# Performance work log

Measured on AMD Instinct MI355X. Metric: run time of the kernel, lower is better.

Reference implementation:

```python
import jax, jax.numpy as jnp
import numpy as np

T = 200000
N_LIMBS = 49
N_POINTS = 50
N_BONES = 20
EPS = 1e-10
REG_RATES = (0.001, 0.1)
# binary-tree skeleton: child b has parent (b-1)//2, bone-length index (b-1)%N_BONES
STRUCTURE = [((b - 1) // 2, b, (b - 1) % N_BONES) for b in range(1, N_POINTS)]

def _path_matrix():
    # P[b, i] = 1 if limb i lies on the root->node-b path. Then node position =
    # root + deltas @ P.T, which is exactly the sequential tree accumulation
    # x[b] = x[a] + delta_i of the original torch loop, vectorized.
    P = np.zeros((N_POINTS, N_LIMBS), dtype=np.float32)
    for i, (a, b, l) in enumerate(STRUCTURE):
        P[b] = P[a]
        P[b, i] = 1.0
    return P

PATH_T = jnp.asarray(_path_matrix().T)  # (n_limbs, n_points)
BONE_IDX = jnp.asarray(np.array([l for (_, _, l) in STRUCTURE], dtype=np.int32))


def setup_inputs() -> dict:
    key = jax.random.key(0)
    ks = jax.random.split(key, 10)
    f = jnp.float32
    return {
        "lines": jax.random.normal(ks[0], (N_BONES,), f) * 0.1,
        "rootsx": jax.random.normal(ks[1], (T, 1), f),
        "rootsy": jax.random.normal(ks[2], (T, 1), f),
        "rootsz": jax.random.normal(ks[3], (T, 1), f),
        "anglesx": jax.random.normal(ks[4], (T, N_LIMBS), f),
        "anglesy": jax.random.normal(ks[5], (T, N_LIMBS), f),
        "anglesz": jax.random.normal(ks[6], (T, N_LIMBS), f),
        "tarx_values": jax.random.normal(ks[7], (T, N_POINTS), f),
        "tary_values": jax.random.normal(ks[8], (T, N_POINTS), f),
        "w_values": jax.random.uniform(ks[9], (T, N_POINTS), f),
    }


def reference(lines, rootsx, rootsy, rootsz, anglesx, anglesy, anglesz,
              tarx_values, tary_values, w_values):
    # per-limb bone length L = exp(lines[l])  -> (n_limbs,)
    L = jnp.exp(lines)[BONE_IDX]
    normA = jnp.sqrt(anglesx ** 2 + anglesy ** 2 + anglesz ** 2) + EPS  # (T, n_limbs)
    dx = L * anglesx / normA
    dy = L * anglesy / normA
    dz = L * anglesz / normA
    # accumulate deltas along root->node paths (equivalent to the torch tree loop)
    x = rootsx + dx @ PATH_T  # (T, n_points); node 0 column is just the root
    y = rootsy + dy @ PATH_T
    z = rootsz + dz @ PATH_T
    loss = jnp.sum(w_values * (x - tarx_values) ** 2
                   + w_values * (y - tary_values) ** 2) / (T * N_POINTS)
    reg1 = jnp.sum(jnp.exp(lines))
    tdx = x[:-1] - x[1:]
    tdy = y[:-1] - y[1:]
    tdz = z[:-1] - z[1:]
    reg2 = jnp.sum(tdx ** 2 + tdy ** 2 + tdz ** 2) / ((T - 1) * N_POINTS)
    total_loss = loss + REG_RATES[0] * reg1 + REG_RATES[1] * reg2
    return x, y, z, total_loss
```

## Files before the change

kernel.cpp:

```cpp
#include <hip/hip_runtime.h>

#define T_TOTAL 200000
#define NL 49
#define NP 50
#define NB 20
#define THREADS 256
#define WPB 4
#define TPW 8
#define NWAVES (T_TOTAL / TPW)
#define NBLOCKS (NWAVES / WPB)
#define REG 456

__global__ __launch_bounds__(THREADS, 5) void bbf_fused(
    const float* __restrict__ lines,
    const float* __restrict__ rootsx,
    const float* __restrict__ rootsy,
    const float* __restrict__ rootsz,
    const float* __restrict__ ax,
    const float* __restrict__ ay,
    const float* __restrict__ az,
    const float* __restrict__ tarx,
    const float* __restrict__ tary,
    const float* __restrict__ w,
    float* __restrict__ outx,
    float* __restrict__ outy,
    float* __restrict__ outz,
    double* __restrict__ partials)
{
    __shared__ __align__(16) float xsW[WPB][REG];
    __shared__ __align__(16) float ysW[WPB][REG];
    __shared__ __align__(16) float zsW[WPB][REG];
    __shared__ double redL[WPB], redR[WPB];

    const int tid  = threadIdx.x;
    const int lane = tid & 63;
    const int wix  = tid >> 6;
    const int gw   = blockIdx.x * WPB + wix;
    const int tw   = __builtin_amdgcn_readfirstlane(gw * TPW);
    const bool lastw = (tw + TPW) >= T_TOTAL;

    const bool isNode = (lane < NP);
    const bool isLimb = (lane >= 1 && lane < NP);
    const int  li = isLimb ? (lane - 1) : 0;

    const float Lv = isLimb ? expf(lines[li % NB]) : 0.f;

    const int a1 = isLimb ? ((lane - 1) >> 1) : 0;
    const int a2 = (a1 > 0) ? ((a1 - 1) >> 1) : 0;
    const int a3 = (a2 > 0) ? ((a2 - 1) >> 1) : 0;
    const int a4 = (a3 > 0) ? ((a3 - 1) >> 1) : 0;

    const float* axp = ax + (size_t)tw * NL + li;
    const float* ayp = ay + (size_t)tw * NL + li;
    const float* azp = az + (size_t)tw * NL + li;
    const size_t o8 = lastw ? (size_t)(7 * NL) : (size_t)(8 * NL);
    float ax0,ay0,az0,ax1,ay1,az1,ax2,ay2,az2,ax3,ay3,az3,ax4,ay4,az4,
          ax5,ay5,az5,ax6,ay6,az6,ax7,ay7,az7,ax8,ay8,az8;
    ax0=axp[0*NL]; ay0=ayp[0*NL]; az0=azp[0*NL];
    ax1=axp[1*NL]; ay1=ayp[1*NL]; az1=azp[1*NL];
    ax2=axp[2*NL]; ay2=ayp[2*NL]; az2=azp[2*NL];
    ax3=axp[3*NL]; ay3=ayp[3*NL]; az3=azp[3*NL];
    ax4=axp[4*NL]; ay4=ayp[4*NL]; az4=azp[4*NL];
    ax5=axp[5*NL]; ay5=ayp[5*NL]; az5=azp[5*NL];
    ax6=axp[6*NL]; ay6=ayp[6*NL]; az6=azp[6*NL];
    ax7=axp[7*NL]; ay7=ayp[7*NL]; az7=azp[7*NL];
    ax8=axp[o8];   ay8=ayp[o8];   az8=azp[o8];
    asm volatile("" ::
        "v"(ax0),"v"(ay0),"v"(az0),"v"(ax1),"v"(ay1),"v"(az1),
        "v"(ax2),"v"(ay2),"v"(az2),"v"(ax3),"v"(ay3),"v"(az3),
        "v"(ax4),"v"(ay4),"v"(az4),"v"(ax5),"v"(ay5),"v"(az5),
        "v"(ax6),"v"(ay6),"v"(az6),"v"(ax7),"v"(ay7),"v"(az7),
        "v"(ax8),"v"(ay8),"v"(az8));

    const int tH = lastw ? (tw + TPW - 1) : (tw + TPW);
    const float rx0=rootsx[tw+0], ry0=rootsy[tw+0], rz0=rootsz[tw+0];
    const float rx1=rootsx[tw+1], ry1=rootsy[tw+1], rz1=rootsz[tw+1];
    const float rx2=rootsx[tw+2], ry2=rootsy[tw+2], rz2=rootsz[tw+2];
    const float rx3=rootsx[tw+3], ry3=rootsy[tw+3], rz3=rootsz[tw+3];
    const float rx4=rootsx[tw+4], ry4=rootsy[tw+4], rz4=rootsz[tw+4];
    const float rx5=rootsx[tw+5], ry5=rootsy[tw+5], rz5=rootsz[tw+5];
    const float rx6=rootsx[tw+6], ry6=rootsy[tw+6], rz6=rootsz[tw+6];
    const float rx7=rootsx[tw+7], ry7=rootsy[tw+7], rz7=rootsz[tw+7];
    const float rx8=rootsx[tH],   ry8=rootsy[tH],   rz8=rootsz[tH];

    float* xw = xsW[wix];
    float* yw = ysW[wix];
    float* zw = zsW[wix];

#define CHAIN(K, AXK, AYK, AZK)                                               \
    {                                                                         \
        const float n = sqrtf(AXK*AXK + AYK*AYK + AZK*AZK) + 1e-10f;          \
        const float s = Lv / n;                                               \
        float dx = AXK * s, dy = AYK * s, dz = AZK * s;                       \
        dx += __shfl(dx, a1); dy += __shfl(dy, a1); dz += __shfl(dz, a1);     \
        dx += __shfl(dx, a2); dy += __shfl(dy, a2); dz += __shfl(dz, a2);     \
        dx += __shfl(dx, a4); dy += __shfl(dy, a4); dz += __shfl(dz, a4);     \
        if (isNode) {                                                         \
            xw[(K)*NP + lane] = dx + rx##K;                                   \
            yw[(K)*NP + lane] = dy + ry##K;                                   \
            zw[(K)*NP + lane] = dz + rz##K;                                   \
        }                                                                     \
    }
    CHAIN(0, ax0, ay0, az0)
    CHAIN(1, ax1, ay1, az1)
    CHAIN(2, ax2, ay2, az2)
    CHAIN(3, ax3, ay3, az3)
    CHAIN(4, ax4, ay4, az4)
    CHAIN(5, ax5, ay5, az5)
    CHAIN(6, ax6, ay6, az6)
    CHAIN(7, ax7, ay7, az7)
    CHAIN(8, ax8, ay8, az8)
#undef CHAIN

    const size_t gb = (size_t)tw * NP;
    const float4* tx4 = (const float4*)(tarx + gb);
    const float4* ty4 = (const float4*)(tary + gb);
    const float4* qw4 = (const float4*)(w + gb);
    float4* ox4 = (float4*)(outx + gb);
    float4* oy4 = (float4*)(outy + gb);
    float4* oz4 = (float4*)(outz + gb);

    float lossAcc = 0.f, regAcc = 0.f;
#pragma unroll
    for (int it = 0; it < 2; ++it) {
        const int c = lane + it * 64;
        if (c < (TPW * NP) / 4) {
            const int j = c << 2;
            const float4 X  = *(const float4*)&xw[j];
            const float4 Y  = *(const float4*)&yw[j];
            const float4 Z  = *(const float4*)&zw[j];
            ox4[c] = X;
            oy4[c] = Y;
            oz4[c] = Z;
            const float4 TX = tx4[c];
            const float4 TY = ty4[c];
            const float4 WV = qw4[c];
            const float4 XA = *(const float4*)&xw[j + 48];
            const float4 XB = *(const float4*)&xw[j + 52];
            const float4 YA = *(const float4*)&yw[j + 48];
            const float4 YB = *(const float4*)&yw[j + 52];
            const float4 ZA = *(const float4*)&zw[j + 48];
            const float4 ZB = *(const float4*)&zw[j + 52];
            const float xv[4] = {X.x, X.y, X.z, X.w};
            const float yv[4] = {Y.x, Y.y, Y.z, Y.w};
            const float zv[4] = {Z.x, Z.y, Z.z, Z.w};
            const float tx[4] = {TX.x, TX.y, TX.z, TX.w};
            const float ty[4] = {TY.x, TY.y, TY.z, TY.w};
            const float qv[4] = {WV.x, WV.y, WV.z, WV.w};
            const float xn[4] = {XA.z, XA.w, XB.x, XB.y};
            const float yn[4] = {YA.z, YA.w, YB.x, YB.y};
            const float zn[4] = {ZA.z, ZA.w, ZB.x, ZB.y};
#pragma unroll
            for (int e = 0; e < 4; ++e) {
                const float ex = xv[e] - tx[e];
                const float ey = yv[e] - ty[e];
                lossAcc += qv[e] * (ex * ex + ey * ey);
                const float d1 = xv[e] - xn[e];
                const float d2 = yv[e] - yn[e];
                const float d3 = zv[e] - zn[e];
                regAcc += d1 * d1 + d2 * d2 + d3 * d3;
            }
        }
    }

    for (int off = 32; off > 0; off >>= 1) {
        lossAcc += __shfl_down(lossAcc, off);
        regAcc  += __shfl_down(regAcc, off);
    }
    if (lane == 0) { redL[wix] = (double)lossAcc; redR[wix] = (double)regAcc; }
    __syncthreads();
    if (tid == 0) {
        double l = 0.0, r = 0.0;
        for (int i = 0; i < WPB; ++i) { l += redL[i]; r += redR[i]; }
        partials[2 * (size_t)blockIdx.x]     = l;
        partials[2 * (size_t)blockIdx.x + 1] = r;
    }
}

__global__ __launch_bounds__(1024) void bbf_finalize(
    const float* __restrict__ lines,
    const double* __restrict__ partials,
    float* __restrict__ out_total)
{
    __shared__ double rl[16], rr[16];
    const int tid = threadIdx.x;
    double l = 0.0, r = 0.0;
    for (int i = tid; i < NBLOCKS; i += 1024) {
        l += partials[2 * (size_t)i];
        r += partials[2 * (size_t)i + 1];
    }
    for (int off = 32; off > 0; off >>= 1) {
        l += __shfl_down(l, off);
        r += __shfl_down(r, off);
    }
    const int wid = tid >> 6;
    if ((tid & 63) == 0) { rl[wid] = l; rr[wid] = r; }
    __syncthreads();
    if (tid == 0) {
        double L = 0.0, R = 0.0;
        for (int i = 0; i < 16; ++i) { L += rl[i]; R += rr[i]; }
        double reg1 = 0.0;
        for (int i = 0; i < NB; ++i) reg1 += (double)expf(lines[i]);
        const double loss = L / ((double)T_TOTAL * (double)NP);
        const double reg2 = R / ((double)(T_TOTAL - 1) * (double)NP);
        *out_total = (float)(loss + 0.001 * reg1 + 0.1 * reg2);
    }
}

extern "C" void kernel_launch(void* const* d_in, const int* in_sizes, int n_in,
                              void* d_out, int out_size, void* d_ws, size_t ws_size,
                              hipStream_t stream) {
    const float* lines  = (const float*)d_in[0];
    const float* rootsx = (const float*)d_in[1];
    const float* rootsy = (const float*)d_in[2];
    const float* rootsz = (const float*)d_in[3];
    const float* ax     = (const float*)d_in[4];
    const float* ay     = (const float*)d_in[5];
    const float* az     = (const float*)d_in[6];
    const float* tarx   = (const float*)d_in[7];
    const float* tary   = (const float*)d_in[8];
    const float* w      = (const float*)d_in[9];

    float* out = (float*)d_out;
    const size_t plane = (size_t)T_TOTAL * NP;
    float* outx = out;
    float* outy = out + plane;
    float* outz = out + 2 * plane;
    float* out_total = out + 3 * plane;

    double* partials = (double*)d_ws;

    bbf_fused<<<NBLOCKS, THREADS, 0, stream>>>(
        lines, rootsx, rootsy, rootsz, ax, ay, az, tarx, tary, w,
        outx, outy, outz, partials);
    bbf_finalize<<<1, 1024, 0, stream>>>(lines, partials, out_total);
}
```

Before: 76.17 us.

## Stage block's angle rows in shared memory via coalesced float4 loads

```diff
diff --git a/kernel.cpp b/kernel.cpp
--- a/kernel.cpp
+++ b/kernel.cpp
@@ -4,14 +4,14 @@
 #define NL 49
 #define NP 50
 #define NB 20
+#define TB 32
 #define THREADS 256
 #define WPB 4
 #define TPW 8
-#define NWAVES (T_TOTAL / TPW)
-#define NBLOCKS (NWAVES / WPB)
-#define REG 456
-
-__global__ __launch_bounds__(THREADS, 5) void bbf_fused(
+#define NBLK (T_TOTAL / TB)
+#define RSTRIDE 456
+
+__global__ __launch_bounds__(THREADS, 6) void bbf_fused(
     const float* __restrict__ lines,
     const float* __restrict__ rootsx,
     const float* __restrict__ rootsy,
@@ -27,17 +27,17 @@
     float* __restrict__ outz,
     double* __restrict__ partials)
 {
-    __shared__ __align__(16) float xsW[WPB][REG];
-    __shared__ __align__(16) float ysW[WPB][REG];
-    __shared__ __align__(16) float zsW[WPB][REG];
+    __shared__ __align__(16) float bx[WPB * RSTRIDE];
+    __shared__ __align__(16) float by[WPB * RSTRIDE];
+    __shared__ __align__(16) float bz[WPB * RSTRIDE];
     __shared__ double redL[WPB], redR[WPB];
 
     const int tid  = threadIdx.x;
     const int lane = tid & 63;
-    const int wix  = tid >> 6;
-    const int gw   = blockIdx.x * WPB + wix;
-    const int tw   = __builtin_amdgcn_readfirstlane(gw * TPW);
-    const bool lastw = (tw + TPW) >= T_TOTAL;
+    const int wv   = tid >> 6;
+    const int t0   = blockIdx.x * TB;
+    const int nrows = min(TB + 1, T_TOTAL - t0);
+    const int nload = nrows * NL;
 
     const bool isNode = (lane < NP);
     const bool isLimb = (lane >= 1 && lane < NP);
@@ -50,69 +50,62 @@
     const int a3 = (a2 > 0) ? ((a2 - 1) >> 1) : 0;
     const int a4 = (a3 > 0) ? ((a3 - 1) >> 1) : 0;
 
-    const float* axp = ax + (size_t)tw * NL + li;
-    const float* ayp = ay + (size_t)tw * NL + li;
-    const float* azp = az + (size_t)tw * NL + li;
-    const size_t o8 = lastw ? (size_t)(7 * NL) : (size_t)(8 * NL);
-    float ax0,ay0,az0,ax1,ay1,az1,ax2,ay2,az2,ax3,ay3,az3,ax4,ay4,az4,
-          ax5,ay5,az5,ax6,ay6,az6,ax7,ay7,az7,ax8,ay8,az8;
-    ax0=axp[0*NL]; ay0=ayp[0*NL]; az0=azp[0*NL];
-    ax1=axp[1*NL]; ay1=ayp[1*NL]; az1=azp[1*NL];
-    ax2=axp[2*NL]; ay2=ayp[2*NL]; az2=azp[2*NL];
-    ax3=axp[3*NL]; ay3=ayp[3*NL]; az3=azp[3*NL];
-    ax4=axp[4*NL]; ay4=ayp[4*NL]; az4=azp[4*NL];
-    ax5=axp[5*NL]; ay5=ayp[5*NL]; az5=azp[5*NL];
-    ax6=axp[6*NL]; ay6=ayp[6*NL]; az6=azp[6*NL];
-    ax7=axp[7*NL]; ay7=ayp[7*NL]; az7=azp[7*NL];
-    ax8=axp[o8];   ay8=ayp[o8];   az8=azp[o8];
-    asm volatile("" ::
-        "v"(ax0),"v"(ay0),"v"(az0),"v"(ax1),"v"(ay1),"v"(az1),
-        "v"(ax2),"v"(ay2),"v"(az2),"v"(ax3),"v"(ay3),"v"(az3),
-        "v"(ax4),"v"(ay4),"v"(az4),"v"(ax5),"v"(ay5),"v"(az5),
-        "v"(ax6),"v"(ay6),"v"(az6),"v"(ax7),"v"(ay7),"v"(az7),
-        "v"(ax8),"v"(ay8),"v"(az8));
-
-    const int tH = lastw ? (tw + TPW - 1) : (tw + TPW);
-    const float rx0=rootsx[tw+0], ry0=rootsy[tw+0], rz0=rootsz[tw+0];
-    const float rx1=rootsx[tw+1], ry1=rootsy[tw+1], rz1=rootsz[tw+1];
-    const float rx2=rootsx[tw+2], ry2=rootsy[tw+2], rz2=rootsz[tw+2];
-    const float rx3=rootsx[tw+3], ry3=rootsy[tw+3], rz3=rootsz[tw+3];
-    const float rx4=rootsx[tw+4], ry4=rootsy[tw+4], rz4=rootsz[tw+4];
-    const float rx5=rootsx[tw+5], ry5=rootsy[tw+5], rz5=rootsz[tw+5];
-    const float rx6=rootsx[tw+6], ry6=rootsy[tw+6], rz6=rootsz[tw+6];
-    const float rx7=rootsx[tw+7], ry7=rootsy[tw+7], rz7=rootsz[tw+7];
-    const float rx8=rootsx[tH],   ry8=rootsy[tH],   rz8=rootsz[tH];
-
-    float* xw = xsW[wix];
-    float* yw = ysW[wix];
-    float* zw = zsW[wix];
-
-#define CHAIN(K, AXK, AYK, AZK)                                               \
-    {                                                                         \
-        const float n = sqrtf(AXK*AXK + AYK*AYK + AZK*AZK) + 1e-10f;          \
-        const float s = Lv / n;                                               \
-        float dx = AXK * s, dy = AYK * s, dz = AZK * s;                       \
-        dx += __shfl(dx, a1); dy += __shfl(dy, a1); dz += __shfl(dz, a1);     \
-        dx += __shfl(dx, a2); dy += __shfl(dy, a2); dz += __shfl(dz, a2);     \
-        dx += __shfl(dx, a4); dy += __shfl(dy, a4); dz += __shfl(dz, a4);     \
-        if (isNode) {                                                         \
-            xw[(K)*NP + lane] = dx + rx##K;                                   \
-            yw[(K)*NP + lane] = dy + ry##K;                                   \
-            zw[(K)*NP + lane] = dz + rz##K;                                   \
-        }                                                                     \
-    }
-    CHAIN(0, ax0, ay0, az0)
-    CHAIN(1, ax1, ay1, az1)
-    CHAIN(2, ax2, ay2, az2)
-    CHAIN(3, ax3, ay3, az3)
-    CHAIN(4, ax4, ay4, az4)
-    CHAIN(5, ax5, ay5, az5)
-    CHAIN(6, ax6, ay6, az6)
-    CHAIN(7, ax7, ay7, az7)
-    CHAIN(8, ax8, ay8, az8)
-#undef CHAIN
-
-    const size_t gb = (size_t)tw * NP;
+    {
+        const float4* ax4 = (const float4*)(ax + (size_t)t0 * NL);
+        const float4* ay4 = (const float4*)(ay + (size_t)t0 * NL);
+        const float4* az4 = (const float4*)(az + (size_t)t0 * NL);
+        const int nv4 = nload >> 2;
+        for (int k4 = tid; k4 < nv4; k4 += THREADS) {
+            ((float4*)bx)[k4] = ax4[k4];
+            ((float4*)by)[k4] = ay4[k4];
+            ((float4*)bz)[k4] = az4[k4];
+        }
+        for (int k = (nload & ~3) + tid; k < nload; k += THREADS) {
+            bx[k] = ax[(size_t)t0 * NL + k];
+            by[k] = ay[(size_t)t0 * NL + k];
+            bz[k] = az[(size_t)t0 * NL + k];
+        }
+    }
+    __syncthreads();
+
+    const int rb = __builtin_amdgcn_readfirstlane(wv * TPW);
+    float arx[9], ary[9], arz[9];
+#pragma unroll
+    for (int k = 0; k < 9; ++k) {
+        const int r = min(rb + k, nrows - 1);
+        const int o = r * NL + li;
+        arx[k] = bx[o];
+        ary[k] = by[o];
+        arz[k] = bz[o];
+    }
+    float rxv[9], ryv[9], rzv[9];
+#pragma unroll
+    for (int k = 0; k < 9; ++k) {
+        const int t = min(t0 + rb + k, T_TOTAL - 1);
+        rxv[k] = rootsx[t]; ryv[k] = rootsy[t]; rzv[k] = rootsz[t];
+    }
+    __syncthreads();
+
+    float* xw = bx + wv * RSTRIDE;
+    float* yw = by + wv * RSTRIDE;
+    float* zw = bz + wv * RSTRIDE;
+#pragma unroll
+    for (int k = 0; k < 9; ++k) {
+        const float x = arx[k], y = ary[k], z = arz[k];
+        const float n = sqrtf(x * x + y * y + z * z) + 1e-10f;
+        const float s = Lv / n;
+        float dx = x * s, dy = y * s, dz = z * s;
+        dx += __shfl(dx, a1); dy += __shfl(dy, a1); dz += __shfl(dz, a1);
+        dx += __shfl(dx, a2); dy += __shfl(dy, a2); dz += __shfl(dz, a2);
+        dx += __shfl(dx, a4); dy += __shfl(dy, a4); dz += __shfl(dz, a4);
+        if (isNode) {
+            xw[k * NP + lane] = dx + rxv[k];
+            yw[k * NP + lane] = dy + ryv[k];
+            zw[k * NP + lane] = dz + rzv[k];
+        }
+    }
+
+    const size_t gb = (size_t)(t0 + rb) * NP;
     const float4* tx4 = (const float4*)(tarx + gb);
     const float4* ty4 = (const float4*)(tary + gb);
     const float4* qw4 = (const float4*)(w + gb);
@@ -167,7 +160,7 @@
         lossAcc += __shfl_down(lossAcc, off);
         regAcc  += __shfl_down(regAcc, off);
     }
-    if (lane == 0) { redL[wix] = (double)lossAcc; redR[wix] = (double)regAcc; }
+    if (lane == 0) { redL[wv] = (double)lossAcc; redR[wv] = (double)regAcc; }
     __syncthreads();
     if (tid == 0) {
         double l = 0.0, r = 0.0;
@@ -185,7 +178,7 @@
     __shared__ double rl[16], rr[16];
     const int tid = threadIdx.x;
     double l = 0.0, r = 0.0;
-    for (int i = tid; i < NBLOCKS; i += 1024) {
+    for (int i = tid; i < NBLK; i += 1024) {
         l += partials[2 * (size_t)i];
         r += partials[2 * (size_t)i + 1];
     }
@@ -230,7 +223,7 @@
 
     double* partials = (double*)d_ws;
 
-    bbf_fused<<<NBLOCKS, THREADS, 0, stream>>>(
+    bbf_fused<<<NBLK, THREADS, 0, stream>>>(
         lines, rootsx, rootsy, rootsz, ax, ay, az, tarx, tary, w,
         outx, outy, outz, partials);
     bbf_finalize<<<1, 1024, 0, stream>>>(lines, partials, out_total);
```

Result: slower. 81.24 us (+6.7%).
